# Kernel optimization log

Measured on AMD Instinct MI355X. Metric: run time of the kernel, lower is better.

Reference implementation:

```python
import jax, jax.numpy as jnp
import numpy as np

D_MODEL = 256; N_HEADS = 8; N_LEVELS = 4; N_POINTS = 4; D_FF = 2048
SHAPES = [(128, 128), (64, 64), (32, 32), (16, 16)]  # (H_l, W_l) per level
LV = sum(h * w for h, w in SHAPES)  # 21760
B = 8; NQ = 900
EPS = 1e-5


def layer_norm(x, s, b):
    m = x.mean(-1, keepdims=True)
    v = x.var(-1, keepdims=True)
    return (x - m) * jax.lax.rsqrt(v + EPS) * s + b


def mha(q, k, v, in_w, in_b, out_w, out_b):
    # torch nn.MultiheadAttention, batch_first, eval mode (no dropout)
    Bq, Lq, C = q.shape
    h = N_HEADS; d = C // h
    wq, wk, wv = jnp.split(in_w, 3, axis=0)
    bq, bk, bv = jnp.split(in_b, 3)
    qh = (q @ wq.T + bq).reshape(Bq, Lq, h, d)
    kh = (k @ wk.T + bk).reshape(Bq, -1, h, d)
    vh = (v @ wv.T + bv).reshape(Bq, -1, h, d)
    scale = jnp.asarray(1.0 / np.sqrt(d), q.dtype)
    attn = jax.nn.softmax(jnp.einsum('bqhd,bkhd->bhqk', qh, kh) * scale, axis=-1)
    o = jnp.einsum('bhqk,bkhd->bqhd', attn, vh).reshape(Bq, Lq, C)
    return o @ out_w.T + out_b


def deform_attn(query, ref, memory, spatial_shapes, val_w, val_b, off_w, off_b, aw_w, aw_b, co_w, co_b):
    # MSDeformAttn forward (eval): offsets/weights from query, bilinear sample value per level/point
    Bq, Lq, C = query.shape
    h, L, P = N_HEADS, N_LEVELS, N_POINTS
    dh = C // h
    value = (memory @ val_w.T + val_b).reshape(Bq, -1, h, dh)  # (B, Lv, h, dh)
    off = (query @ off_w.T + off_b).reshape(Bq, Lq, h, L, P, 2)
    aw = jax.nn.softmax((query @ aw_w.T + aw_b).reshape(Bq, Lq, h, L * P), axis=-1)
    aw = aw.reshape(Bq, Lq, h, L, P)
    # normalizer = (W_l, H_l) per level
    normalizer = spatial_shapes[:, ::-1].astype(query.dtype)
    loc = ref[:, :, None, :, None, :] + off / normalizer[None, None, None, :, None, :]  # (B,Lq,h,L,P,2)
    out = jnp.zeros((Bq, h, Lq, dh), query.dtype)
    start = 0
    for l, (Hl, Wl) in enumerate(SHAPES):
        v_l = value[:, start:start + Hl * Wl].transpose(0, 2, 1, 3)  # (B,h,Hl*Wl,dh)
        start += Hl * Wl
        xy = loc[:, :, :, l]  # (B,Lq,h,P,2) normalized in [0,1]
        # grid_sample align_corners=False pixel coords
        x = xy[..., 0] * Wl - 0.5
        y = xy[..., 1] * Hl - 0.5
        x0 = jnp.floor(x); y0 = jnp.floor(y)
        wx = x - x0; wy = y - y0
        acc = jnp.zeros((Bq, h, Lq * P, dh), query.dtype)
        for dx, dy, w in ((0, 0, (1 - wx) * (1 - wy)), (1, 0, wx * (1 - wy)),
                          (0, 1, (1 - wx) * wy), (1, 1, wx * wy)):
            xi = x0 + dx; yi = y0 + dy
            valid = (xi >= 0) & (xi <= Wl - 1) & (yi >= 0) & (yi <= Hl - 1)
            xi = jnp.clip(xi, 0, Wl - 1).astype(jnp.int32)
            yi = jnp.clip(yi, 0, Hl - 1).astype(jnp.int32)
            idx = (yi * Wl + xi).transpose(0, 2, 1, 3).reshape(Bq, h, Lq * P)
            g = jnp.take_along_axis(v_l, idx[..., None], axis=2)  # (B,h,Lq*P,dh)
            wgt = (w * valid).transpose(0, 2, 1, 3).reshape(Bq, h, Lq * P)
            acc = acc + g * wgt[..., None]
        acc = acc.reshape(Bq, h, Lq, P, dh)
        wl = aw[:, :, :, l].transpose(0, 2, 1, 3)  # (B,h,Lq,P)
        out = out + jnp.einsum('bhqpd,bhqp->bhqd', acc, wl)
    out = out.transpose(0, 2, 1, 3).reshape(Bq, Lq, C)
    return out @ co_w.T + co_b


def forward(tgt, memory, query_pos, reference_points, sa_in_w, sa_in_b, sa_out_w, sa_out_b,
            off_w, off_b, aw_w, aw_b, val_w, val_b, co_w, co_b,
            l1_w, l1_b, l2_w, l2_b, ln1_s, ln1_b, ln2_s, ln2_b, ln3_s, ln3_b, spatial_shapes):
    q = tgt + query_pos  # with_pos_embed; eval mode: no group_detr split, no dropout
    tgt2 = mha(q, q, tgt, sa_in_w, sa_in_b, sa_out_w, sa_out_b)
    tgt = layer_norm(tgt + tgt2, ln1_s, ln1_b)
    tgt2 = deform_attn(tgt + query_pos, reference_points, memory, spatial_shapes,
                       val_w, val_b, off_w, off_b, aw_w, aw_b, co_w, co_b)
    tgt = layer_norm(tgt + tgt2, ln2_s, ln2_b)
    tgt2 = jax.nn.relu(tgt @ l1_w.T + l1_b) @ l2_w.T + l2_b
    return layer_norm(tgt + tgt2, ln3_s, ln3_b)


def setup_inputs():
    key = jax.random.key(0)
    ks = jax.random.split(key, 16)
    C = D_MODEL
    f = lambda i, shape, s=0.02: jax.random.normal(ks[i], shape, jnp.float32) * s
    HLP = N_HEADS * N_LEVELS * N_POINTS
    return {
        'tgt': f(0, (B, NQ, C), 1.0),
        'memory': f(1, (B, LV, C), 1.0),
        'query_pos': f(2, (B, NQ, C), 1.0),
        'reference_points': jax.random.uniform(ks[3], (B, NQ, N_LEVELS, 2), jnp.float32),
        'sa_in_w': f(4, (3 * C, C)), 'sa_in_b': jnp.zeros((3 * C,), jnp.float32),
        'sa_out_w': f(5, (C, C)), 'sa_out_b': jnp.zeros((C,), jnp.float32),
        'off_w': f(6, (HLP * 2, C)), 'off_b': f(7, (HLP * 2,), 0.5),
        'aw_w': f(8, (HLP, C)), 'aw_b': jnp.zeros((HLP,), jnp.float32),
        'val_w': f(9, (C, C)), 'val_b': jnp.zeros((C,), jnp.float32),
        'co_w': f(10, (C, C)), 'co_b': jnp.zeros((C,), jnp.float32),
        'l1_w': f(11, (D_FF, C)), 'l1_b': jnp.zeros((D_FF,), jnp.float32),
        'l2_w': f(12, (C, D_FF)), 'l2_b': jnp.zeros((C,), jnp.float32),
        'ln1_s': jnp.ones((C,), jnp.float32), 'ln1_b': jnp.zeros((C,), jnp.float32),
        'ln2_s': jnp.ones((C,), jnp.float32), 'ln2_b': jnp.zeros((C,), jnp.float32),
        'ln3_s': jnp.ones((C,), jnp.float32), 'ln3_b': jnp.zeros((C,), jnp.float32),
        'spatial_shapes': jnp.asarray(SHAPES, jnp.int32),
        'level_start_index': jnp.asarray(np.cumsum([0] + [h * w for h, w in SHAPES[:-1]]), jnp.int32),
    }


def reference(tgt, memory, query_pos, reference_points, sa_in_w, sa_in_b, sa_out_w, sa_out_b,
              off_w, off_b, aw_w, aw_b, val_w, val_b, co_w, co_b,
              l1_w, l1_b, l2_w, l2_b, ln1_s, ln1_b, ln2_s, ln2_b, ln3_s, ln3_b,
              spatial_shapes, level_start_index):
    return forward(tgt, memory, query_pos, reference_points, sa_in_w, sa_in_b, sa_out_w, sa_out_b,
                   off_w, off_b, aw_w, aw_b, val_w, val_b, co_w, co_b,
                   l1_w, l1_b, l2_w, l2_b, ln1_s, ln1_b, ln2_s, ln2_b, ln3_s, ln3_b, spatial_shapes)
```

## Files before the change

kernel.cpp:

```cpp
#include <hip/hip_runtime.h>
#include <hip/hip_bf16.h>

#define NQL 900
#define CDIM 256
#define BDIM 8
#define LVTOT 21760

typedef __bf16 bf16x8 __attribute__((ext_vector_type(8)));
typedef float f32x4 __attribute__((ext_vector_type(4)));
typedef uint u32x4 __attribute__((ext_vector_type(4)));
typedef uint u32x2 __attribute__((ext_vector_type(2)));

__device__ __forceinline__ ushort f2bf(float x) {
  uint u = __builtin_bit_cast(uint, x);
  u += 0x7fff + ((u >> 16) & 1);
  return (ushort)(u >> 16);
}

template <bool ABF16, bool AADD, bool RELU, bool HASRES, bool OUTBF16>
__global__ __launch_bounds__(256, 2) void mgemm_kernel(const void* __restrict__ Ap,
                                                       const float* __restrict__ A2p,
                                                       const float* __restrict__ W,
                                                       const float* __restrict__ bias,
                                                       const float* __restrict__ Rres,
                                                       void* __restrict__ Cout,
                                                       int M, int N, int K) {
  __shared__ ushort smem[17408];
  ushort* As = smem;
  ushort* Bs = smem + 5120;
  const int tid = threadIdx.x;
  const int m0 = blockIdx.y * 128, n0 = blockIdx.x * 128;
  const int wv = tid >> 6;
  const int wm = (wv >> 1) * 64, wn = (wv & 1) * 64;
  const int lane = tid & 63;
  const int lr = lane & 15, kq = lane >> 4;

  f32x4 acc[4][4] = {};

  float4 pa[2][2], pb[2][2];
  u32x4 pa16[2];

  auto load_tiles = [&](int k0) {
#pragma unroll
    for (int it = 0; it < 2; ++it) {
      int idx = it * 256 + tid;
      int r = idx >> 2, s = (idx & 3) << 3;
      int gm = min(m0 + r, M - 1);
      if constexpr (ABF16) {
        pa16[it] = *(const u32x4*)((const ushort*)Ap + (size_t)gm * K + k0 + s);
      } else {
        const float* ap = (const float*)Ap + (size_t)gm * K + k0 + s;
        pa[it][0] = *(const float4*)ap;
        pa[it][1] = *(const float4*)(ap + 4);
        if constexpr (AADD) {
          const float* ap2 = A2p + (size_t)gm * K + k0 + s;
          float4 q0 = *(const float4*)ap2;
          float4 q1 = *(const float4*)(ap2 + 4);
          pa[it][0].x += q0.x; pa[it][0].y += q0.y; pa[it][0].z += q0.z; pa[it][0].w += q0.w;
          pa[it][1].x += q1.x; pa[it][1].y += q1.y; pa[it][1].z += q1.z; pa[it][1].w += q1.w;
        }
      }
      int gn = min(n0 + r, N - 1);
      const float* wp = W + (size_t)gn * K + k0 + s;
      pb[it][0] = *(const float4*)wp;
      pb[it][1] = *(const float4*)(wp + 4);
    }
  };

  auto store_tiles = [&]() {
#pragma unroll
    for (int it = 0; it < 2; ++it) {
      int idx = it * 256 + tid;
      int r = idx >> 2, s = (idx & 3) << 3;
      u32x4 u;
      if constexpr (ABF16) {
        u = pa16[it];
      } else {
        u.x = f2bf(pa[it][0].x) | ((uint)f2bf(pa[it][0].y) << 16);
        u.y = f2bf(pa[it][0].z) | ((uint)f2bf(pa[it][0].w) << 16);
        u.z = f2bf(pa[it][1].x) | ((uint)f2bf(pa[it][1].y) << 16);
        u.w = f2bf(pa[it][1].z) | ((uint)f2bf(pa[it][1].w) << 16);
      }
      *(u32x4*)&As[r * 40 + s] = u;
      u32x4 w;
      w.x = f2bf(pb[it][0].x) | ((uint)f2bf(pb[it][0].y) << 16);
      w.y = f2bf(pb[it][0].z) | ((uint)f2bf(pb[it][0].w) << 16);
      w.z = f2bf(pb[it][1].x) | ((uint)f2bf(pb[it][1].y) << 16);
      w.w = f2bf(pb[it][1].z) | ((uint)f2bf(pb[it][1].w) << 16);
      *(u32x4*)&Bs[r * 40 + s] = w;
    }
  };

  load_tiles(0);
  for (int k0 = 0; k0 < K; k0 += 32) {
    store_tiles();
    __syncthreads();
    if (k0 + 32 < K) load_tiles(k0 + 32);
    bf16x8 af[4], bq[4];
#pragma unroll
    for (int m = 0; m < 4; ++m)
      af[m] = __builtin_bit_cast(bf16x8, *(const u32x4*)&As[(wm + m * 16 + lr) * 40 + kq * 8]);
#pragma unroll
    for (int n = 0; n < 4; ++n)
      bq[n] = __builtin_bit_cast(bf16x8, *(const u32x4*)&Bs[(wn + n * 16 + lr) * 40 + kq * 8]);
#pragma unroll
    for (int m = 0; m < 4; ++m)
#pragma unroll
      for (int n = 0; n < 4; ++n)
        acc[m][n] = __builtin_amdgcn_mfma_f32_16x16x32_bf16(af[m], bq[n], acc[m][n], 0, 0, 0);
    __syncthreads();
  }

  if constexpr (OUTBF16) {
    ushort* Cs = smem;
#pragma unroll
    for (int n = 0; n < 4; ++n) {
      int col = wn + n * 16 + lr;
      float bv = bias[n0 + col];
#pragma unroll
      for (int m = 0; m < 4; ++m) {
#pragma unroll
        for (int j = 0; j < 4; ++j) {
          int row = wm + m * 16 + kq * 4 + j;
          float v = acc[m][n][j] + bv;
          if (RELU) v = fmaxf(v, 0.f);
          Cs[row * 136 + col] = f2bf(v);
        }
      }
    }
    __syncthreads();
#pragma unroll
    for (int p = 0; p < 8; ++p) {
      int row = p * 16 + (tid >> 4);
      int grow = m0 + row;
      if (grow < M) {
        u32x4 u = *(const u32x4*)&Cs[row * 136 + (tid & 15) * 8];
        *(u32x4*)((ushort*)Cout + (size_t)grow * N + n0 + (tid & 15) * 8) = u;
      }
    }
  } else {
#pragma unroll
    for (int n = 0; n < 4; ++n) {
      int gcol = n0 + wn + n * 16 + lr;
      float bv = bias[gcol];
#pragma unroll
      for (int m = 0; m < 4; ++m) {
        int rbase = m0 + wm + m * 16 + kq * 4;
#pragma unroll
        for (int j = 0; j < 4; ++j) {
          int grow = rbase + j;
          if (grow >= M) continue;
          float v = acc[m][n][j] + bv;
          if (HASRES) v += Rres[(size_t)grow * N + gcol];
          if (RELU) v = fmaxf(v, 0.f);
          ((float*)Cout)[(size_t)grow * N + gcol] = v;
        }
      }
    }
  }
}

__global__ __launch_bounds__(256) void vt_kernel(const ushort* __restrict__ tmp_v,
                                                 ushort* __restrict__ vt) {
  __shared__ ushort Ls[64 * 40];
  const int qt = blockIdx.x;
  const int bh = blockIdx.y;
  const int b = bh >> 3, h = bh & 7;
  const int tid = threadIdx.x;
  const int q0 = qt * 64;
  {
    int r = tid >> 2, c = (tid & 3) * 8;
    int gq = min(q0 + r, NQL - 1);
    u32x4 u = *(const u32x4*)(tmp_v + ((size_t)(b * NQL + gq) * 256) + h * 32 + c);
    *(u32x4*)&Ls[r * 40 + c] = u;
  }
  __syncthreads();
  {
    int d = tid >> 3, qw = (tid & 7) * 8;
    u32x4 u;
    uint w[8];
#pragma unroll
    for (int j = 0; j < 8; ++j) w[j] = Ls[(qw + j) * 40 + d];
    u.x = w[0] | (w[1] << 16);
    u.y = w[2] | (w[3] << 16);
    u.z = w[4] | (w[5] << 16);
    u.w = w[6] | (w[7] << 16);
    *(u32x4*)(vt + ((size_t)(bh * 32 + d) * 960) + q0 + qw) = u;
  }
}

__global__ __launch_bounds__(256, 2) void fattn_kernel(const ushort* __restrict__ qk,
                                                       const ushort* __restrict__ vt,
                                                       float* __restrict__ out) {
  __shared__ ushort Ks[64 * 40];
  __shared__ ushort Vs[32 * 72];
  __shared__ ushort Ps[4][16 * 72];
  const int qt = blockIdx.x, bh = blockIdx.y;
  const int b = bh >> 3, h = bh & 7;
  const int tid = threadIdx.x;
  const int wv = tid >> 6, lane = tid & 63;
  const int lq = lane & 15, hi = lane >> 4;
  const int q0 = qt * 64 + wv * 16;
  const float SC = 0.17677669529663689f;

  bf16x8 qfrag;
  {
    int qrow = min(q0 + lq, NQL - 1);
    qfrag = __builtin_bit_cast(bf16x8,
        *(const u32x4*)(qk + (size_t)(b * NQL + qrow) * 512 + h * 32 + hi * 8));
  }

  f32x4 o0 = {}, o1 = {};
  float mrow = -1e30f, lrow = 0.f;

  for (int kt = 0; kt < 15; ++kt) {
    const int k0 = kt * 64;
    __syncthreads();
    {
      int r = tid >> 2, c = (tid & 3) * 8;
      int gk = min(k0 + r, NQL - 1);
      u32x4 u = *(const u32x4*)(qk + (size_t)(b * NQL + gk) * 512 + 256 + h * 32 + c);
      *(u32x4*)&Ks[r * 40 + c] = u;
    }
    {
      int r = tid >> 3, c = (tid & 7) * 8;
      u32x4 u = *(const u32x4*)(vt + (size_t)(bh * 32 + r) * 960 + k0 + c);
      *(u32x4*)&Vs[r * 72 + c] = u;
    }
    __syncthreads();

    f32x4 st[4];
#pragma unroll
    for (int mt = 0; mt < 4; ++mt) {
      bf16x8 kf = __builtin_bit_cast(bf16x8, *(const u32x4*)&Ks[(mt * 16 + lq) * 40 + hi * 8]);
      f32x4 z = {};
      st[mt] = __builtin_amdgcn_mfma_f32_16x16x32_bf16(kf, qfrag, z, 0, 0, 0);
    }
    float sv[4][4];
    float lmax = -1e30f;
#pragma unroll
    for (int mt = 0; mt < 4; ++mt)
#pragma unroll
      for (int j = 0; j < 4; ++j) {
        int key = k0 + mt * 16 + hi * 4 + j;
        float v = st[mt][j] * SC;
        v = (key < NQL) ? v : -1e30f;
        sv[mt][j] = v;
        lmax = fmaxf(lmax, v);
      }
    lmax = fmaxf(lmax, __shfl_xor(lmax, 16));
    lmax = fmaxf(lmax, __shfl_xor(lmax, 32));
    float mnew = fmaxf(mrow, lmax);
    float rs = __expf(mrow - mnew);
    float lsum = 0.f;
    uint pw[4][2];
#pragma unroll
    for (int mt = 0; mt < 4; ++mt) {
      float p0 = __expf(sv[mt][0] - mnew);
      float p1 = __expf(sv[mt][1] - mnew);
      float p2 = __expf(sv[mt][2] - mnew);
      float p3 = __expf(sv[mt][3] - mnew);
      lsum += (p0 + p1) + (p2 + p3);
      pw[mt][0] = f2bf(p0) | ((uint)f2bf(p1) << 16);
      pw[mt][1] = f2bf(p2) | ((uint)f2bf(p3) << 16);
    }
    lsum += __shfl_xor(lsum, 16);
    lsum += __shfl_xor(lsum, 32);
    lrow = lrow * rs + lsum;
    mrow = mnew;
#pragma unroll
    for (int j = 0; j < 4; ++j) {
      float rsj = __shfl(rs, hi * 4 + j);
      o0[j] *= rsj;
      o1[j] *= rsj;
    }
#pragma unroll
    for (int mt = 0; mt < 4; ++mt) {
      u32x2 u;
      u.x = pw[mt][0];
      u.y = pw[mt][1];
      *(u32x2*)&Ps[wv][lq * 72 + mt * 16 + hi * 4] = u;
    }
#pragma unroll
    for (int k2 = 0; k2 < 2; ++k2) {
      bf16x8 pa = __builtin_bit_cast(bf16x8, *(const u32x4*)&Ps[wv][lq * 72 + k2 * 32 + hi * 8]);
      bf16x8 vb0 = __builtin_bit_cast(bf16x8, *(const u32x4*)&Vs[(0 * 16 + lq) * 72 + k2 * 32 + hi * 8]);
      bf16x8 vb1 = __builtin_bit_cast(bf16x8, *(const u32x4*)&Vs[(1 * 16 + lq) * 72 + k2 * 32 + hi * 8]);
      o0 = __builtin_amdgcn_mfma_f32_16x16x32_bf16(pa, vb0, o0, 0, 0, 0);
      o1 = __builtin_amdgcn_mfma_f32_16x16x32_bf16(pa, vb1, o1, 0, 0, 0);
    }
  }

#pragma unroll
  for (int j = 0; j < 4; ++j) {
    float lj = __shfl(lrow, hi * 4 + j);
    float inv = 1.f / lj;
    int gq = q0 + hi * 4 + j;
    if (gq < NQL) {
      float* op = out + (size_t)(b * NQL + gq) * 256 + h * 32;
      op[lq] = o0[j] * inv;
      op[16 + lq] = o1[j] * inv;
    }
  }
}

__global__ __launch_bounds__(256) void ln_kernel(const float* __restrict__ x,
                                                 const float* __restrict__ s,
                                                 const float* __restrict__ bb,
                                                 float* __restrict__ out) {
  int row = blockIdx.x, tid = threadIdx.x;
  float v = x[(size_t)row * 256 + tid];
  __shared__ float r1[256], r2[256];
  r1[tid] = v;
  r2[tid] = v * v;
  __syncthreads();
  for (int st = 128; st > 0; st >>= 1) {
    if (tid < st) { r1[tid] += r1[tid + st]; r2[tid] += r2[tid + st]; }
    __syncthreads();
  }
  float m = r1[0] * (1.f / 256);
  float var = r2[0] * (1.f / 256) - m * m;
  out[(size_t)row * 256 + tid] = (v - m) * rsqrtf(var + 1e-5f) * s[tid] + bb[tid];
}

__global__ __launch_bounds__(128) void awsm_kernel(float* __restrict__ aw) {
  int row = blockIdx.x, tid = threadIdx.x;
  float v = aw[(size_t)row * 128 + tid];
  float m = v;
  for (int d = 1; d < 16; d <<= 1) m = fmaxf(m, __shfl_xor(m, d));
  float e = expf(v - m);
  float ssum = e;
  for (int d = 1; d < 16; d <<= 1) ssum += __shfl_xor(ssum, d);
  aw[(size_t)row * 128 + tid] = e / ssum;
}

__global__ __launch_bounds__(256) void deform_kernel(const __hip_bfloat16* __restrict__ value,
                                                     const float* __restrict__ offb,
                                                     const float* __restrict__ awb,
                                                     const float* __restrict__ refp,
                                                     float* __restrict__ dfout) {
  const int Hs[4] = {128, 64, 32, 16};
  const int Stl[4] = {0, 16384, 20480, 21504};
  int row = blockIdx.x;
  int b = row / NQL;
  int tid = threadIdx.x;
  int h = tid >> 5, d = tid & 31;
  const float* off = offb + (size_t)row * 256;
  const float* aw = awb + (size_t)row * 128;
  const float* ref = refp + (size_t)row * 8;
  const __hip_bfloat16* vb = value + (size_t)b * LVTOT * 256 + h * 32 + d;
  float acc = 0.f;
#pragma unroll
  for (int l = 0; l < 4; ++l) {
    int Wi = Hs[l], Hi = Hs[l];
    float Wl = (float)Wi, Hl = (float)Hi;
    int st = Stl[l];
    float rx = ref[l * 2 + 0], ry = ref[l * 2 + 1];
#pragma unroll
    for (int p = 0; p < 4; ++p) {
      int oi = ((h * 4 + l) * 4 + p) * 2;
      float x = (rx + off[oi] / Wl) * Wl - 0.5f;
      float y = (ry + off[oi + 1] / Hl) * Hl - 0.5f;
      float w = aw[h * 16 + l * 4 + p];
      float x0f = floorf(x), y0f = floorf(y);
      float wx = x - x0f, wy = y - y0f;
      int xi0 = (int)x0f, yi0 = (int)y0f;
      float samp = 0.f;
#pragma unroll
      for (int dy = 0; dy < 2; ++dy) {
#pragma unroll
        for (int dx = 0; dx < 2; ++dx) {
          int xi = xi0 + dx, yi = yi0 + dy;
          float tw = (dx ? wx : 1.f - wx) * (dy ? wy : 1.f - wy);
          bool valid = (xi >= 0) && (xi < Wi) && (yi >= 0) && (yi < Hi);
          int xc = min(max(xi, 0), Wi - 1);
          int yc = min(max(yi, 0), Hi - 1);
          float vv = __bfloat162float(vb[(size_t)(st + yc * Wi + xc) * 256]);
          samp += valid ? tw * vv : 0.f;
        }
      }
      acc = fmaf(w, samp, acc);
    }
  }
  dfout[(size_t)row * 256 + tid] = acc;
}

extern "C" void kernel_launch(void* const* d_in, const int* in_sizes, int n_in,
                              void* d_out, int out_size, void* d_ws, size_t ws_size,
                              hipStream_t stream) {
  const float* tgt = (const float*)d_in[0];
  const float* memory = (const float*)d_in[1];
  const float* qpos = (const float*)d_in[2];
  const float* refp = (const float*)d_in[3];
  const float* sa_in_w = (const float*)d_in[4];
  const float* sa_in_b = (const float*)d_in[5];
  const float* sa_out_w = (const float*)d_in[6];
  const float* sa_out_b = (const float*)d_in[7];
  const float* off_w = (const float*)d_in[8];
  const float* off_b = (const float*)d_in[9];
  const float* aw_w = (const float*)d_in[10];
  const float* aw_b = (const float*)d_in[11];
  const float* val_w = (const float*)d_in[12];
  const float* val_b = (const float*)d_in[13];
  const float* co_w = (const float*)d_in[14];
  const float* co_b = (const float*)d_in[15];
  const float* l1_w = (const float*)d_in[16];
  const float* l1_b = (const float*)d_in[17];
  const float* l2_w = (const float*)d_in[18];
  const float* l2_b = (const float*)d_in[19];
  const float* ln1_s = (const float*)d_in[20];
  const float* ln1_b = (const float*)d_in[21];
  const float* ln2_s = (const float*)d_in[22];
  const float* ln2_b = (const float*)d_in[23];
  const float* ln3_s = (const float*)d_in[24];
  const float* ln3_b = (const float*)d_in[25];

  float* ws = (float*)d_ws;
  const size_t E = (size_t)BDIM * NQL * CDIM;
  ushort* vt = (ushort*)(ws + E);
  float* attn_o = ws + 4 * E;
  ushort* tmp_qk = (ushort*)(ws + 5 * E);
  ushort* tmp_v = (ushort*)(ws + 7 * E);
  float* sa_out = ws + 5 * E;
  float* offb = ws + E;
  float* awb = ws + 2 * E;
  float* dfout = ws + 3 * E;
  float* co_out = ws + 4 * E;
  ushort* hidden = (ushort*)ws;
  float* tgt1 = ws + 8 * E;
  float* tgt2 = ws + 9 * E;
  float* ffn_o = ws + 10 * E;
  ushort* valbf = (ushort*)(ws + 11 * E);

  const int M = BDIM * NQL;
  const int MT = (M + 127) / 128;
  dim3 blk(256);

  mgemm_kernel<false, true, false, false, true><<<dim3(4, MT), blk, 0, stream>>>(
      tgt, qpos, sa_in_w, sa_in_b, nullptr, tmp_qk, M, 512, 256);
  mgemm_kernel<false, false, false, false, true><<<dim3(2, MT), blk, 0, stream>>>(
      tgt, nullptr, sa_in_w + 512 * 256, sa_in_b + 512, nullptr, tmp_v, M, 256, 256);
  vt_kernel<<<dim3(15, 64), blk, 0, stream>>>(tmp_v, vt);
  fattn_kernel<<<dim3(15, 64), blk, 0, stream>>>(tmp_qk, vt, attn_o);
  mgemm_kernel<false, false, false, true, false><<<dim3(2, MT), blk, 0, stream>>>(
      attn_o, nullptr, sa_out_w, sa_out_b, tgt, sa_out, M, 256, 256);
  ln_kernel<<<M, blk, 0, stream>>>(sa_out, ln1_s, ln1_b, tgt1);
  mgemm_kernel<false, false, false, false, true><<<dim3(2, (BDIM * LVTOT) / 128), blk, 0, stream>>>(
      memory, nullptr, val_w, val_b, nullptr, valbf, BDIM * LVTOT, 256, 256);
  mgemm_kernel<false, true, false, false, false><<<dim3(2, MT), blk, 0, stream>>>(
      tgt1, qpos, off_w, off_b, nullptr, offb, M, 256, 256);
  mgemm_kernel<false, true, false, false, false><<<dim3(1, MT), blk, 0, stream>>>(
      tgt1, qpos, aw_w, aw_b, nullptr, awb, M, 128, 256);
  awsm_kernel<<<M, 128, 0, stream>>>(awb);
  deform_kernel<<<M, blk, 0, stream>>>((const __hip_bfloat16*)valbf, offb, awb, refp, dfout);
  mgemm_kernel<false, false, false, true, false><<<dim3(2, MT), blk, 0, stream>>>(
      dfout, nullptr, co_w, co_b, tgt1, co_out, M, 256, 256);
  ln_kernel<<<M, blk, 0, stream>>>(co_out, ln2_s, ln2_b, tgt2);
  mgemm_kernel<false, false, true, false, true><<<dim3(16, MT), blk, 0, stream>>>(
      tgt2, nullptr, l1_w, l1_b, nullptr, hidden, M, 2048, 256);
  mgemm_kernel<true, false, false, true, false><<<dim3(2, MT), blk, 0, stream>>>(
      hidden, nullptr, l2_w, l2_b, tgt2, ffn_o, M, 256, 2048);
  ln_kernel<<<M, blk, 0, stream>>>(ffn_o, ln3_s, ln3_b, (float*)d_out);
}
```

Measured before the change: 409.7 us.

## Add full-width 64x256 GEMM with fused residual+LayerNorm epilogue, shrink mgemm LDS

Adds a GEMM kernel that computes a full 256-column row tile (64 rows per block), so bias, residual add and LayerNorm run in the epilogue and the three standalone LayerNorm kernels plus their intermediate buffers go away. The value projection, V projection and offset projection also move to this kernel. The original 128x128 GEMM writes its bf16 output in two 64-row halves, which cuts its shared memory and lets the launch bound allow 4 blocks per SM. The trade-off is that each full-width block reloads and converts the whole 256-row weight tile for every K step, and the LN epilogue keeps many values live in registers.

```diff
diff --git a/kernel.cpp b/kernel.cpp
--- a/kernel.cpp
+++ b/kernel.cpp
@@ -17,15 +17,14 @@
   return (ushort)(u >> 16);
 }
 
-template <bool ABF16, bool AADD, bool RELU, bool HASRES, bool OUTBF16>
-__global__ __launch_bounds__(256, 2) void mgemm_kernel(const void* __restrict__ Ap,
+template <bool ABF16, bool AADD, bool RELU, bool OUTBF16>
+__global__ __launch_bounds__(256, 4) void mgemm_kernel(const void* __restrict__ Ap,
                                                        const float* __restrict__ A2p,
                                                        const float* __restrict__ W,
                                                        const float* __restrict__ bias,
-                                                       const float* __restrict__ Rres,
                                                        void* __restrict__ Cout,
                                                        int M, int N, int K) {
-  __shared__ ushort smem[17408];
+  __shared__ ushort smem[10240];
   ushort* As = smem;
   ushort* Bs = smem + 5120;
   const int tid = threadIdx.x;
@@ -36,7 +35,6 @@
   const int lr = lane & 15, kq = lane >> 4;
 
   f32x4 acc[4][4] = {};
-
   float4 pa[2][2], pb[2][2];
   u32x4 pa16[2];
 
@@ -114,28 +112,33 @@
   if constexpr (OUTBF16) {
     ushort* Cs = smem;
 #pragma unroll
-    for (int n = 0; n < 4; ++n) {
-      int col = wn + n * 16 + lr;
-      float bv = bias[n0 + col];
-#pragma unroll
-      for (int m = 0; m < 4; ++m) {
-#pragma unroll
-        for (int j = 0; j < 4; ++j) {
-          int row = wm + m * 16 + kq * 4 + j;
-          float v = acc[m][n][j] + bv;
-          if (RELU) v = fmaxf(v, 0.f);
-          Cs[row * 136 + col] = f2bf(v);
+    for (int p = 0; p < 2; ++p) {
+      __syncthreads();
+      if (wm == p * 64) {
+#pragma unroll
+        for (int n = 0; n < 4; ++n) {
+          int col = wn + n * 16 + lr;
+          float bv = bias[n0 + col];
+#pragma unroll
+          for (int m = 0; m < 4; ++m)
+#pragma unroll
+            for (int j = 0; j < 4; ++j) {
+              float v = acc[m][n][j] + bv;
+              if (RELU) v = fmaxf(v, 0.f);
+              Cs[(m * 16 + kq * 4 + j) * 136 + col] = f2bf(v);
+            }
         }
       }
-    }
-    __syncthreads();
-#pragma unroll
-    for (int p = 0; p < 8; ++p) {
-      int row = p * 16 + (tid >> 4);
-      int grow = m0 + row;
-      if (grow < M) {
-        u32x4 u = *(const u32x4*)&Cs[row * 136 + (tid & 15) * 8];
-        *(u32x4*)((ushort*)Cout + (size_t)grow * N + n0 + (tid & 15) * 8) = u;
+      __syncthreads();
+#pragma unroll
+      for (int it = 0; it < 4; ++it) {
+        int idx = it * 256 + tid;
+        int r = idx >> 4, c = (idx & 15) * 8;
+        int grow = m0 + p * 64 + r;
+        if (grow < M) {
+          u32x4 u = *(const u32x4*)&Cs[r * 136 + c];
+          *(u32x4*)((ushort*)Cout + (size_t)grow * N + n0 + c) = u;
+        }
       }
     }
   } else {
@@ -151,10 +154,184 @@
           int grow = rbase + j;
           if (grow >= M) continue;
           float v = acc[m][n][j] + bv;
-          if (HASRES) v += Rres[(size_t)grow * N + gcol];
           if (RELU) v = fmaxf(v, 0.f);
           ((float*)Cout)[(size_t)grow * N + gcol] = v;
         }
+      }
+    }
+  }
+}
+
+template <bool ABF16, bool AADD, bool LNFUSE, bool OUTBF16>
+__global__ __launch_bounds__(256, 2) void mgemm256_kernel(const void* __restrict__ Ap,
+                                                          const float* __restrict__ A2p,
+                                                          const float* __restrict__ W,
+                                                          const float* __restrict__ bias,
+                                                          const float* __restrict__ Rres,
+                                                          const float* __restrict__ lns,
+                                                          const float* __restrict__ lnb,
+                                                          void* __restrict__ Cout,
+                                                          int M, int K) {
+  __shared__ ushort smem[16896];
+  ushort* As = smem;
+  ushort* Bs = smem + 2560;
+  const int tid = threadIdx.x;
+  const int m0 = blockIdx.x * 64;
+  const int wv = tid >> 6;
+  const int lane = tid & 63;
+  const int lr = lane & 15, kq = lane >> 4;
+
+  f32x4 acc[16] = {};
+  float4 pa[2];
+  u32x4 pa16;
+  float4 pb[4][2];
+
+  auto load_tiles = [&](int k0) {
+    {
+      int r = tid >> 2, s = (tid & 3) << 3;
+      int gm = min(m0 + r, M - 1);
+      if constexpr (ABF16) {
+        pa16 = *(const u32x4*)((const ushort*)Ap + (size_t)gm * K + k0 + s);
+      } else {
+        const float* ap = (const float*)Ap + (size_t)gm * K + k0 + s;
+        pa[0] = *(const float4*)ap;
+        pa[1] = *(const float4*)(ap + 4);
+        if constexpr (AADD) {
+          const float* ap2 = A2p + (size_t)gm * K + k0 + s;
+          float4 q0 = *(const float4*)ap2;
+          float4 q1 = *(const float4*)(ap2 + 4);
+          pa[0].x += q0.x; pa[0].y += q0.y; pa[0].z += q0.z; pa[0].w += q0.w;
+          pa[1].x += q1.x; pa[1].y += q1.y; pa[1].z += q1.z; pa[1].w += q1.w;
+        }
+      }
+    }
+#pragma unroll
+    for (int it = 0; it < 4; ++it) {
+      int idx = it * 256 + tid;
+      int r = idx >> 2, s = (idx & 3) << 3;
+      const float* wp = W + (size_t)r * K + k0 + s;
+      pb[it][0] = *(const float4*)wp;
+      pb[it][1] = *(const float4*)(wp + 4);
+    }
+  };
+
+  auto store_tiles = [&]() {
+    {
+      int r = tid >> 2, s = (tid & 3) << 3;
+      u32x4 u;
+      if constexpr (ABF16) {
+        u = pa16;
+      } else {
+        u.x = f2bf(pa[0].x) | ((uint)f2bf(pa[0].y) << 16);
+        u.y = f2bf(pa[0].z) | ((uint)f2bf(pa[0].w) << 16);
+        u.z = f2bf(pa[1].x) | ((uint)f2bf(pa[1].y) << 16);
+        u.w = f2bf(pa[1].z) | ((uint)f2bf(pa[1].w) << 16);
+      }
+      *(u32x4*)&As[r * 40 + s] = u;
+    }
+#pragma unroll
+    for (int it = 0; it < 4; ++it) {
+      int idx = it * 256 + tid;
+      int r = idx >> 2, s = (idx & 3) << 3;
+      u32x4 w;
+      w.x = f2bf(pb[it][0].x) | ((uint)f2bf(pb[it][0].y) << 16);
+      w.y = f2bf(pb[it][0].z) | ((uint)f2bf(pb[it][0].w) << 16);
+      w.z = f2bf(pb[it][1].x) | ((uint)f2bf(pb[it][1].y) << 16);
+      w.w = f2bf(pb[it][1].z) | ((uint)f2bf(pb[it][1].w) << 16);
+      *(u32x4*)&Bs[r * 40 + s] = w;
+    }
+  };
+
+  load_tiles(0);
+  for (int k0 = 0; k0 < K; k0 += 32) {
+    store_tiles();
+    __syncthreads();
+    if (k0 + 32 < K) load_tiles(k0 + 32);
+    bf16x8 af = __builtin_bit_cast(bf16x8, *(const u32x4*)&As[(wv * 16 + lr) * 40 + kq * 8]);
+#pragma unroll
+    for (int ng = 0; ng < 4; ++ng) {
+      bf16x8 b0 = __builtin_bit_cast(bf16x8, *(const u32x4*)&Bs[((ng * 4 + 0) * 16 + lr) * 40 + kq * 8]);
+      bf16x8 b1 = __builtin_bit_cast(bf16x8, *(const u32x4*)&Bs[((ng * 4 + 1) * 16 + lr) * 40 + kq * 8]);
+      bf16x8 b2 = __builtin_bit_cast(bf16x8, *(const u32x4*)&Bs[((ng * 4 + 2) * 16 + lr) * 40 + kq * 8]);
+      bf16x8 b3 = __builtin_bit_cast(bf16x8, *(const u32x4*)&Bs[((ng * 4 + 3) * 16 + lr) * 40 + kq * 8]);
+      acc[ng * 4 + 0] = __builtin_amdgcn_mfma_f32_16x16x32_bf16(af, b0, acc[ng * 4 + 0], 0, 0, 0);
+      acc[ng * 4 + 1] = __builtin_amdgcn_mfma_f32_16x16x32_bf16(af, b1, acc[ng * 4 + 1], 0, 0, 0);
+      acc[ng * 4 + 2] = __builtin_amdgcn_mfma_f32_16x16x32_bf16(af, b2, acc[ng * 4 + 2], 0, 0, 0);
+      acc[ng * 4 + 3] = __builtin_amdgcn_mfma_f32_16x16x32_bf16(af, b3, acc[ng * 4 + 3], 0, 0, 0);
+    }
+    __syncthreads();
+  }
+
+  if constexpr (LNFUSE) {
+    float bv[16], lsv[16], lbv[16];
+#pragma unroll
+    for (int nf = 0; nf < 16; ++nf) {
+      int col = nf * 16 + lr;
+      bv[nf] = bias[col];
+      lsv[nf] = lns[col];
+      lbv[nf] = lnb[col];
+    }
+#pragma unroll
+    for (int j = 0; j < 4; ++j) {
+      int grow = m0 + wv * 16 + kq * 4 + j;
+      int rr = min(grow, M - 1);
+      float x[16];
+      float s1 = 0.f, s2 = 0.f;
+#pragma unroll
+      for (int nf = 0; nf < 16; ++nf) {
+        float v = acc[nf][j] + bv[nf] + Rres[(size_t)rr * 256 + nf * 16 + lr];
+        x[nf] = v;
+        s1 += v;
+        s2 += v * v;
+      }
+#pragma unroll
+      for (int w = 1; w < 16; w <<= 1) {
+        s1 += __shfl_xor(s1, w);
+        s2 += __shfl_xor(s2, w);
+      }
+      float mean = s1 * (1.f / 256.f);
+      float var = s2 * (1.f / 256.f) - mean * mean;
+      float inv = rsqrtf(var + 1e-5f);
+      if (grow < M) {
+        float* op = (float*)Cout + (size_t)grow * 256;
+#pragma unroll
+        for (int nf = 0; nf < 16; ++nf)
+          op[nf * 16 + lr] = (x[nf] - mean) * inv * lsv[nf] + lbv[nf];
+      }
+    }
+  } else if constexpr (OUTBF16) {
+    ushort* Cs = smem;
+#pragma unroll
+    for (int nf = 0; nf < 16; ++nf) {
+      int col = nf * 16 + lr;
+      float bv = bias[col];
+#pragma unroll
+      for (int j = 0; j < 4; ++j) {
+        int row = wv * 16 + kq * 4 + j;
+        Cs[row * 264 + col] = f2bf(acc[nf][j] + bv);
+      }
+    }
+    __syncthreads();
+#pragma unroll
+    for (int it = 0; it < 8; ++it) {
+      int idx = it * 256 + tid;
+      int r = idx >> 5, c = (idx & 31) * 8;
+      int grow = m0 + r;
+      if (grow < M) {
+        u32x4 u = *(const u32x4*)&Cs[r * 264 + c];
+        *(u32x4*)((ushort*)Cout + (size_t)grow * 256 + c) = u;
+      }
+    }
+  } else {
+#pragma unroll
+    for (int nf = 0; nf < 16; ++nf) {
+      int col = nf * 16 + lr;
+      float bv = bias[col];
+#pragma unroll
+      for (int j = 0; j < 4; ++j) {
+        int grow = m0 + wv * 16 + kq * 4 + j;
+        if (grow < M)
+          ((float*)Cout)[(size_t)grow * 256 + col] = acc[nf][j] + bv;
       }
     }
   }
@@ -302,25 +479,6 @@
       op[16 + lq] = o1[j] * inv;
     }
   }
-}
-
-__global__ __launch_bounds__(256) void ln_kernel(const float* __restrict__ x,
-                                                 const float* __restrict__ s,
-                                                 const float* __restrict__ bb,
-                                                 float* __restrict__ out) {
-  int row = blockIdx.x, tid = threadIdx.x;
-  float v = x[(size_t)row * 256 + tid];
-  __shared__ float r1[256], r2[256];
-  r1[tid] = v;
-  r2[tid] = v * v;
-  __syncthreads();
-  for (int st = 128; st > 0; st >>= 1) {
-    if (tid < st) { r1[tid] += r1[tid + st]; r2[tid] += r2[tid + st]; }
-    __syncthreads();
-  }
-  float m = r1[0] * (1.f / 256);
-  float var = r2[0] * (1.f / 256) - m * m;
-  out[(size_t)row * 256 + tid] = (v - m) * rsqrtf(var + 1e-5f) * s[tid] + bb[tid];
 }
 
 __global__ __launch_bounds__(128) void awsm_kernel(float* __restrict__ aw) {
@@ -421,44 +579,39 @@
   float* attn_o = ws + 4 * E;
   ushort* tmp_qk = (ushort*)(ws + 5 * E);
   ushort* tmp_v = (ushort*)(ws + 7 * E);
-  float* sa_out = ws + 5 * E;
   float* offb = ws + E;
   float* awb = ws + 2 * E;
   float* dfout = ws + 3 * E;
-  float* co_out = ws + 4 * E;
   ushort* hidden = (ushort*)ws;
   float* tgt1 = ws + 8 * E;
   float* tgt2 = ws + 9 * E;
-  float* ffn_o = ws + 10 * E;
   ushort* valbf = (ushort*)(ws + 11 * E);
 
   const int M = BDIM * NQL;
   const int MT = (M + 127) / 128;
+  const int M64 = (M + 63) / 64;
   dim3 blk(256);
 
-  mgemm_kernel<false, true, false, false, true><<<dim3(4, MT), blk, 0, stream>>>(
-      tgt, qpos, sa_in_w, sa_in_b, nullptr, tmp_qk, M, 512, 256);
-  mgemm_kernel<false, false, false, false, true><<<dim3(2, MT), blk, 0, stream>>>(
-      tgt, nullptr, sa_in_w + 512 * 256, sa_in_b + 512, nullptr, tmp_v, M, 256, 256);
+  mgemm_kernel<false, true, false, true><<<dim3(4, MT), blk, 0, stream>>>(
+      tgt, qpos, sa_in_w, sa_in_b, tmp_qk, M, 512, 256);
+  mgemm256_kernel<false, false, false, true><<<M64, blk, 0, stream>>>(
+      tgt, nullptr, sa_in_w + 512 * 256, sa_in_b + 512, nullptr, nullptr, nullptr, tmp_v, M, 256);
   vt_kernel<<<dim3(15, 64), blk, 0, stream>>>(tmp_v, vt);
   fattn_kernel<<<dim3(15, 64), blk, 0, stream>>>(tmp_qk, vt, attn_o);
-  mgemm_kernel<false, false, false, true, false><<<dim3(2, MT), blk, 0, stream>>>(
-      attn_o, nullptr, sa_out_w, sa_out_b, tgt, sa_out, M, 256, 256);
-  ln_kernel<<<M, blk, 0, stream>>>(sa_out, ln1_s, ln1_b, tgt1);
-  mgemm_kernel<false, false, false, false, true><<<dim3(2, (BDIM * LVTOT) / 128), blk, 0, stream>>>(
-      memory, nullptr, val_w, val_b, nullptr, valbf, BDIM * LVTOT, 256, 256);
-  mgemm_kernel<false, true, false, false, false><<<dim3(2, MT), blk, 0, stream>>>(
-      tgt1, qpos, off_w, off_b, nullptr, offb, M, 256, 256);
-  mgemm_kernel<false, true, false, false, false><<<dim3(1, MT), blk, 0, stream>>>(
-      tgt1, qpos, aw_w, aw_b, nullptr, awb, M, 128, 256);
+  mgemm256_kernel<false, false, true, false><<<M64, blk, 0, stream>>>(
+      attn_o, nullptr, sa_out_w, sa_out_b, tgt, ln1_s, ln1_b, tgt1, M, 256);
+  mgemm256_kernel<false, false, false, true><<<(BDIM * LVTOT) / 64, blk, 0, stream>>>(
+      memory, nullptr, val_w, val_b, nullptr, nullptr, nullptr, valbf, BDIM * LVTOT, 256);
+  mgemm256_kernel<false, true, false, false><<<M64, blk, 0, stream>>>(
+      tgt1, qpos, off_w, off_b, nullptr, nullptr, nullptr, offb, M, 256);
+  mgemm_kernel<false, true, false, false><<<dim3(1, MT), blk, 0, stream>>>(
+      tgt1, qpos, aw_w, aw_b, awb, M, 128, 256);
   awsm_kernel<<<M, 128, 0, stream>>>(awb);
   deform_kernel<<<M, blk, 0, stream>>>((const __hip_bfloat16*)valbf, offb, awb, refp, dfout);
-  mgemm_kernel<false, false, false, true, false><<<dim3(2, MT), blk, 0, stream>>>(
-      dfout, nullptr, co_w, co_b, tgt1, co_out, M, 256, 256);
-  ln_kernel<<<M, blk, 0, stream>>>(co_out, ln2_s, ln2_b, tgt2);
-  mgemm_kernel<false, false, true, false, true><<<dim3(16, MT), blk, 0, stream>>>(
-      tgt2, nullptr, l1_w, l1_b, nullptr, hidden, M, 2048, 256);
-  mgemm_kernel<true, false, false, true, false><<<dim3(2, MT), blk, 0, stream>>>(
-      hidden, nullptr, l2_w, l2_b, tgt2, ffn_o, M, 256, 2048);
-  ln_kernel<<<M, blk, 0, stream>>>(ffn_o, ln3_s, ln3_b, (float*)d_out);
-}
+  mgemm256_kernel<false, false, true, false><<<M64, blk, 0, stream>>>(
+      dfout, nullptr, co_w, co_b, tgt1, ln2_s, ln2_b, tgt2, M, 256);
+  mgemm_kernel<false, false, true, true><<<dim3(16, MT), blk, 0, stream>>>(
+      tgt2, nullptr, l1_w, l1_b, hidden, M, 2048, 256);
+  mgemm256_kernel<true, false, true, false><<<M64, blk, 0, stream>>>(
+      hidden, nullptr, l2_w, l2_b, tgt2, ln3_s, ln3_b, (float*)d_out, M, 2048);
+}
```

New measurement: 417.0 us. About the same (+1.8%).
